# Performance work log

Hardware: AMD Instinct MI355X
Metric: run time of the kernel (lower is better)

## Reference

```python
import jax, jax.numpy as jnp
import numpy as np

B, C, K, P, H, W = 4, 128, 64, 8, 256, 256


def _img2patch(x, p):
    b, c, h, w = x.shape
    # [b,c,h,w] -> [b,c,p*p, (h//p)*(w//p)]
    return x.reshape(b, c, p, h // p, p, w // p).transpose(0, 1, 2, 4, 3, 5).reshape(b, c, p * p, -1)


def _patch2img(x, p, h, w):
    b, c = x.shape[:2]
    return x.reshape(b, c, p, p, h // p, w // p).transpose(0, 1, 2, 4, 3, 5).reshape(b, c, h, w)


def _conv1x1(x, Wm, bvec=None):
    # 1x1 conv on [b,c,pp,L] == channel matmul
    y = jnp.einsum('oc,bcpl->bopl', Wm, x)
    if bvec is not None:
        y = y + bvec[None, :, None, None]
    return y


def _l2norm(x, axis):
    return x / (1e-6 + jnp.sqrt(jnp.sum(x * x, axis=axis, keepdims=True)))


def setup_inputs():
    key = jax.random.key(0)
    ks = jax.random.split(key, 14)
    def wmat(k_, o, i):
        return jax.random.normal(k_, (o, i), jnp.float32) * np.float32(np.sqrt(2.0 / o))
    def bvec(k_, o):
        return jax.random.normal(k_, (o,), jnp.float32) * np.float32(0.01)
    return {
        'x1': jax.random.normal(ks[0], (B, C, H, W), jnp.float32),
        'x2': jax.random.normal(ks[1], (B, C, H, W), jnp.float32),
        'w_v': wmat(ks[2], K, 2 * C), 'b_v': bvec(ks[3], K),
        'w1_1': wmat(ks[4], C, C), 'b1_1': bvec(ks[5], C),
        'w2_1': wmat(ks[6], K, C), 'b2_1': bvec(ks[7], K),
        'w_out1': wmat(ks[8], C, C),
        'w1_2': wmat(ks[9], C, C), 'b1_2': bvec(ks[10], C),
        'w2_2': wmat(ks[11], K, C), 'b2_2': bvec(ks[12], K),
        'w_out2': wmat(ks[13], C, C),
        'p': P, 'k': K,
    }


def reference(x1, x2, w_v, b_v, w1_1, b1_1, w2_1, b2_1, w_out1, w1_2, b1_2, w2_2, b2_2, w_out2, p, k):
    b, c, h, w = x1.shape
    pp = p * p
    L = (h // p) * (w // p)
    bpp = b * pp
    x1p = _img2patch(x1, p)  # [b,c,pp,L]
    x2p = _img2patch(x2, p)
    y1_1 = _conv1x1(x1p, w1_1, b1_1).transpose(0, 2, 1, 3).reshape(bpp, c, L)
    y2_1 = _conv1x1(x1p, w2_1, b2_1).transpose(0, 2, 3, 1).reshape(bpp, L, k)
    y1_2 = _conv1x1(x2p, w1_2, b1_2).transpose(0, 2, 1, 3).reshape(bpp, c, L)
    y2_2 = _conv1x1(x2p, w2_2, b2_2).transpose(0, 2, 3, 1).reshape(bpp, L, k)
    v = _conv1x1(jnp.concatenate([x1p, x2p], axis=1), w_v, b_v)  # [b,k,pp,L]
    v = v.transpose(0, 2, 1, 3).reshape(bpp, k, L)
    v = jax.nn.softmax(v, axis=1)
    u1 = _l2norm(jnp.matmul(y1_1, y2_1), axis=1)  # [bpp,c,k]
    u2 = _l2norm(jnp.matmul(y1_2, y2_2), axis=1)
    y3_1 = jnp.matmul(u1, v).reshape(b, pp, c, L).transpose(0, 2, 1, 3)
    y3_2 = jnp.matmul(u2, v).reshape(b, pp, c, L).transpose(0, 2, 1, 3)
    out1 = jnp.einsum('oc,bchw->bohw', w_out1, _patch2img(y3_1, p, h, w))
    out2 = jnp.einsum('oc,bchw->bohw', w_out2, _patch2img(y3_2, p, h, w))
    return out1, out2
```

## Files before the change

kernel.cpp:

```cpp
#include <hip/hip_runtime.h>
#include <cstdint>

typedef __attribute__((ext_vector_type(8))) short short8;
typedef __attribute__((ext_vector_type(4))) float v4f;

#define B_ 4
#define C_ 128
#define K_ 64
#define H_ 256
#define W_ 256
#define HW_ (H_*W_)
#define L_ 1024
#define J_ 256
#define LC 128
#define NCH 8

#define OFF_WFH  0ull
#define OFF_WFL  131072ull
#define OFF_WOF  262144ull
#define OFF_BIAS 327680ull
#define OFF_VWS  335872ull
#define OFF_MFR  (OFF_VWS + 33554432ull)

static __device__ __forceinline__ unsigned short f2bf(float x) {
    unsigned u = __builtin_bit_cast(unsigned, x);
    unsigned r = (u + 0x7FFFu + ((u >> 16) & 1u)) >> 16;
    return (unsigned short)r;
}
static __device__ __forceinline__ float bf2f(unsigned short h) {
    unsigned u = ((unsigned)h) << 16;
    return __builtin_bit_cast(float, u);
}
static __device__ __forceinline__ v4f mfma16(short8 a, short8 b, v4f c) {
    return __builtin_amdgcn_mfma_f32_16x16x32_bf16(a, b, c, 0, 0, 0);
}

union U8 { unsigned short u[8]; short8 v; };

__global__ void prep_kernel(const float* __restrict__ w_v, const float* __restrict__ b_v,
                            const float* __restrict__ w1_1, const float* __restrict__ b1_1,
                            const float* __restrict__ w2_1, const float* __restrict__ b2_1,
                            const float* __restrict__ wout1,
                            const float* __restrict__ w1_2, const float* __restrict__ b1_2,
                            const float* __restrict__ w2_2, const float* __restrict__ b2_2,
                            const float* __restrict__ wout2,
                            char* __restrict__ wsb) {
    int tid = blockIdx.x * 256 + threadIdx.x;
    if (tid < 65536) {
        int jj = tid & 7, lane = (tid >> 3) & 63, kc = (tid >> 9) & 3;
        int omt = (tid >> 11) & 15, s = (tid >> 15) & 1;
        int o = omt * 16 + (lane & 15);
        int c = kc * 32 + ((lane >> 4) * 8) + jj;
        const float* w1 = s ? w1_2 : w1_1;
        const float* w2 = s ? w2_2 : w2_1;
        float v;
        if (o < 128)      v = w1[o * 128 + c];
        else if (o < 192) v = w2[(o - 128) * 128 + c];
        else              v = w_v[(o - 192) * 256 + s * 128 + c];
        unsigned short hi = f2bf(v);
        unsigned short lo = f2bf(v - bf2f(hi));
        ((unsigned short*)(wsb + OFF_WFH))[tid] = hi;
        ((unsigned short*)(wsb + OFF_WFL))[tid] = lo;
    } else if (tid < 98304) {
        int id = tid - 65536;
        int jj = id & 7, lane = (id >> 3) & 63, kc = (id >> 9) & 3;
        int om = (id >> 11) & 7, s = (id >> 14) & 1;
        int o = om * 16 + (lane & 15);
        int c = kc * 32 + ((lane >> 4) * 8) + jj;
        const float* wo = s ? wout2 : wout1;
        ((unsigned short*)(wsb + OFF_WOF))[id] = f2bf(wo[o * 128 + c]);
    } else if (tid < 98816) {
        int id = tid - 98304;
        int s = id >> 8, o = id & 255;
        const float* b1 = s ? b1_2 : b1_1;
        const float* b2 = s ? b2_2 : b2_1;
        float v;
        if (o < 128)      v = b1[o];
        else if (o < 192) v = b2[o - 128];
        else              v = b_v[o - 192];
        ((float*)(wsb + OFF_BIAS))[id] = v;
    }
}

__global__ __attribute__((amdgpu_flat_work_group_size(512, 512), amdgpu_waves_per_eu(2, 2)))
void fused_kernel(
    const float* __restrict__ x1, const float* __restrict__ x2,
    char* __restrict__ wsb) {
    __shared__ __align__(16) char smem[151040];
    unsigned short* Xfh = (unsigned short*)&smem[0];
    unsigned short* Xfl = (unsigned short*)&smem[32768];
    unsigned short* Y1b = (unsigned short*)&smem[65536];
    unsigned short* Y2b = (unsigned short*)&smem[100352];
    float*          LG  = (float*)&smem[117760];
    float*          UF  = (float*)&smem[0];
    unsigned short* UH  = (unsigned short*)&smem[100352];
    unsigned short* MB  = (unsigned short*)&smem[65536];

    const unsigned short* wfh = (const unsigned short*)(wsb + OFF_WFH);
    const unsigned short* wfl = (const unsigned short*)(wsb + OFF_WFL);
    const unsigned short* wof = (const unsigned short*)(wsb + OFF_WOF);
    const float* biasws = (const float*)(wsb + OFF_BIAS);
    unsigned short* vws = (unsigned short*)(wsb + OFF_VWS);
    unsigned short* mfr = (unsigned short*)(wsb + OFF_MFR);

    const int t = threadIdx.x;
    const int lane = t & 63;
    const int w = __builtin_amdgcn_readfirstlane(t >> 6);
    const int j = blockIdx.x;
    const int b = j >> 6, q = j & 63, i0 = q >> 3, i2 = q & 7;
    const long imgbase = (long)b * C_ * HW_ + (long)(i0 * 32) * W_ + i2 * 32;

    const int lquad = lane >> 4;
    const int lmod = lane & 15;

    float pb[2][2][4];
#pragma unroll
    for (int s = 0; s < 2; s++)
#pragma unroll
        for (int h = 0; h < 2; h++)
#pragma unroll
            for (int r = 0; r < 4; r++)
                pb[s][h][r] = biasws[s * 256 + w * 32 + h * 16 + lquad * 4 + r];

    v4f uacc[2][4];
#pragma unroll
    for (int s = 0; s < 2; s++)
#pragma unroll
        for (int kn = 0; kn < 4; kn++)
            uacc[s][kn] = (v4f){0.f, 0.f, 0.f, 0.f};

    const int dl = t & 127, c8 = t >> 7;
    const int srow = dl >> 5, scol = dl & 31;
    const int sln = dl >> 4, slp = dl & 15;

    float R[32];
#pragma unroll
    for (int p = 0; p < 4; p++)
#pragma unroll
        for (int jj = 0; jj < 8; jj++) {
            int c = (p * 4 + c8) * 8 + jj;
            R[p * 8 + jj] = x1[imgbase + (long)c * HW_ + srow * W_ + scol];
        }

    for (int lc = 0; lc < NCH; lc++) {
        v4f pacc[2][8];
#pragma unroll
        for (int s = 0; s < 2; s++) {
#pragma unroll
            for (int p = 0; p < 4; p++) {
                U8 hv, lv;
#pragma unroll
                for (int jj = 0; jj < 8; jj++) {
                    float v = R[p * 8 + jj];
                    unsigned short hh = f2bf(v);
                    hv.u[jj] = hh;
                    lv.u[jj] = f2bf(v - bf2f(hh));
                }
                int co = p * 4 + c8;
                int base = ((sln * 4 + (co >> 2)) * 64 + ((co & 3) * 16 + slp)) * 8;
                *(short8*)&Xfh[base] = hv.v;
                *(short8*)&Xfl[base] = lv.v;
            }
            __syncthreads();
            if (s == 0 || lc < NCH - 1) {
                const float* xp = s ? x1 : x2;
                const int nlc = s ? lc + 1 : lc;
#pragma unroll
                for (int p = 0; p < 4; p++)
#pragma unroll
                    for (int jj = 0; jj < 8; jj++) {
                        int c = (p * 4 + c8) * 8 + jj;
                        R[p * 8 + jj] = xp[imgbase + (long)c * HW_ + (nlc * 4 + srow) * W_ + scol];
                    }
            }
            if (s == 0 || w < 6) {
#pragma unroll
                for (int h = 0; h < 2; h++)
#pragma unroll
                    for (int ln = 0; ln < 8; ln++)
                        pacc[h][ln] = (v4f){pb[s][h][0], pb[s][h][1], pb[s][h][2], pb[s][h][3]};
            }
#pragma unroll
            for (int kc = 0; kc < 4; kc++) {
                int wi0 = (((s * 16 + (w * 2 + 0)) * 4 + kc) * 64 + lane) * 8;
                int wi1 = (((s * 16 + (w * 2 + 1)) * 4 + kc) * 64 + lane) * 8;
                short8 wh0 = *(const short8*)&wfh[wi0];
                short8 wh1 = *(const short8*)&wfh[wi1];
                short8 wlo0 = *(const short8*)&wfl[wi0];
                short8 wlo1 = *(const short8*)&wfl[wi1];
#pragma unroll
                for (int ln = 0; ln < 8; ln++) {
                    short8 bh = *(const short8*)&Xfh[((ln * 4 + kc) * 64 + lane) * 8];
                    short8 bl = *(const short8*)&Xfl[((ln * 4 + kc) * 64 + lane) * 8];
                    pacc[0][ln] = mfma16(wh0, bh, pacc[0][ln]);
                    pacc[0][ln] = mfma16(wlo0, bh, pacc[0][ln]);
                    pacc[0][ln] = mfma16(wh0, bl, pacc[0][ln]);
                    pacc[1][ln] = mfma16(wh1, bh, pacc[1][ln]);
                    pacc[1][ln] = mfma16(wlo1, bh, pacc[1][ln]);
                    pacc[1][ln] = mfma16(wh1, bl, pacc[1][ln]);
                }
            }
            if (w < 4) {
#pragma unroll
                for (int h = 0; h < 2; h++)
#pragma unroll
                    for (int ln = 0; ln < 8; ln++)
#pragma unroll
                        for (int r = 0; r < 4; r++)
                            Y1b[(w * 32 + h * 16 + lquad * 4 + r) * 136 + ln * 16 + lmod] = f2bf(pacc[h][ln][r]);
            } else if (w < 6) {
#pragma unroll
                for (int h = 0; h < 2; h++)
#pragma unroll
                    for (int ln = 0; ln < 8; ln++)
#pragma unroll
                        for (int r = 0; r < 4; r++)
                            Y2b[((w - 4) * 32 + h * 16 + lquad * 4 + r) * 136 + ln * 16 + lmod] = f2bf(pacc[h][ln][r]);
            } else if (s == 1) {
#pragma unroll
                for (int h = 0; h < 2; h++)
#pragma unroll
                    for (int ln = 0; ln < 8; ln++)
#pragma unroll
                        for (int r = 0; r < 4; r++)
                            LG[(ln * 16 + lmod) * 65 + (w - 6) * 32 + h * 16 + lquad * 4 + r] = pacc[h][ln][r];
            }
            __syncthreads();
#pragma unroll
            for (int kcl = 0; kcl < 4; kcl++) {
                short8 a = *(const short8*)&Y1b[(w * 16 + lmod) * 136 + kcl * 32 + lquad * 8];
#pragma unroll
                for (int kn = 0; kn < 4; kn++) {
                    short8 bb = *(const short8*)&Y2b[(kn * 16 + lmod) * 136 + kcl * 32 + lquad * 8];
                    uacc[s][kn] = mfma16(a, bb, uacc[s][kn]);
                }
            }
            if (s == 1) {
                if (t < 128) {
                    float* row = &LG[t * 65];
                    float mx = row[0];
#pragma unroll 8
                    for (int k = 1; k < 64; k++) mx = fmaxf(mx, row[k]);
                    float ssum = 0.f;
#pragma unroll 8
                    for (int k = 0; k < 64; k++) { float e = __expf(row[k] - mx); row[k] = e; ssum += e; }
                    float rs = 1.f / ssum;
#pragma unroll 8
                    for (int k = 0; k < 64; k++) row[k] *= rs;
                }
                __syncthreads();
                {
                    int l2 = t >> 2, kq = (t & 3) * 16;
                    U8 o1, o2;
#pragma unroll
                    for (int i = 0; i < 8; i++) o1.u[i] = f2bf(LG[l2 * 65 + kq + i]);
#pragma unroll
                    for (int i = 0; i < 8; i++) o2.u[i] = f2bf(LG[l2 * 65 + kq + 8 + i]);
                    unsigned long long vb = ((unsigned long long)j * 1024 + lc * 128 + l2) * 64 + kq;
                    *(short8*)&vws[vb] = o1.v;
                    *(short8*)&vws[vb + 8] = o2.v;
                }
            }
        }
    }

#pragma unroll
    for (int s = 0; s < 2; s++) {
        __syncthreads();
#pragma unroll
        for (int kn = 0; kn < 4; kn++)
#pragma unroll
            for (int r = 0; r < 4; r++)
                UF[(kn * 16 + lmod) * 133 + w * 16 + lquad * 4 + r] = uacc[s][kn][r];
        __syncthreads();
        if (t < 64) {
            const float* rp = &UF[t * 133];
            float ss = 0.f;
#pragma unroll 8
            for (int c = 0; c < 128; c++) ss += rp[c] * rp[c];
            UF[t * 133 + 128] = 1.f / (1e-6f + sqrtf(ss));
        }
        __syncthreads();
        {
            int kk = t >> 3, c0 = (t & 7) * 16;
            float rn = UF[kk * 133 + 128];
#pragma unroll
            for (int i = 0; i < 16; i++)
                UH[kk * 136 + c0 + i] = f2bf(UF[kk * 133 + c0 + i] * rn);
        }
        __syncthreads();
        v4f macc[4];
#pragma unroll
        for (int kn = 0; kn < 4; kn++) macc[kn] = (v4f){0.f, 0.f, 0.f, 0.f};
#pragma unroll
        for (int kc = 0; kc < 4; kc++) {
            short8 a = *(const short8*)&wof[(((s * 8 + w) * 4 + kc) * 64 + lane) * 8];
#pragma unroll
            for (int kn = 0; kn < 4; kn++) {
                short8 bb = *(const short8*)&UH[(kn * 16 + lmod) * 136 + kc * 32 + lquad * 8];
                macc[kn] = mfma16(a, bb, macc[kn]);
            }
        }
        __syncthreads();
#pragma unroll
        for (int kn = 0; kn < 4; kn++)
#pragma unroll
            for (int r = 0; r < 4; r++)
                MB[(w * 16 + lquad * 4 + r) * 72 + kn * 16 + lmod] = f2bf(macc[kn][r]);
        __syncthreads();
#pragma unroll
        for (int p = 0; p < 2; p++) {
            int id = p * 512 + t;
            int om = id >> 7, kc = (id >> 6) & 1, l2 = id & 63;
            short8 mv = *(const short8*)&MB[(om * 16 + (l2 & 15)) * 72 + kc * 32 + ((l2 >> 4) * 8)];
            *(short8*)&mfr[(((unsigned long long)j * 2 + s) * 1024 + id) * 8] = mv;
        }
    }
}

__global__ __launch_bounds__(512, 4) void out_kernel(const char* __restrict__ wsb,
                                                     float* __restrict__ out) {
    const unsigned short* vws = (const unsigned short*)(wsb + OFF_VWS);
    const unsigned short* mfr = (const unsigned short*)(wsb + OFF_MFR);
    const int t = threadIdx.x;
    const int lane = t & 63;
    const int w = __builtin_amdgcn_readfirstlane(t >> 6);
    const int j = blockIdx.x >> 2;
    const int slice = blockIdx.x & 3;
    const int b = j >> 6, q = j & 63, i0 = q >> 3, i2 = q & 7;
    const long obase = (long)b * C_ * HW_ + (long)(i0 * 32) * W_ + i2 * 32;
    const int lquad = lane >> 4, lmod = lane & 15;

    short8 afr[2][2];
#pragma unroll
    for (int s = 0; s < 2; s++)
#pragma unroll
        for (int kc = 0; kc < 2; kc++)
            afr[s][kc] = *(const short8*)&mfr[(((unsigned long long)j * 2 + s) * 1024 + (w * 2 + kc) * 64 + lane) * 8];

    const long orow = obase + (long)(w * 16 + lmod) * HW_;
#pragma unroll 4
    for (int i = 0; i < 16; i++) {
        int ln = slice * 16 + i;
        int l = ln * 16 + lmod;
        short8 b0  = *(const short8*)&vws[((unsigned long long)j * 1024 + l) * 64 + lquad * 8];
        short8 b1v = *(const short8*)&vws[((unsigned long long)j * 1024 + l) * 64 + 32 + lquad * 8];
        int lo = ln * 16 + lquad * 4;
        long base2 = orow + (long)(lo >> 5) * W_ + (lo & 31);
#pragma unroll
        for (int s = 0; s < 2; s++) {
            v4f acc = {0.f, 0.f, 0.f, 0.f};
            acc = mfma16(b0,  afr[s][0], acc);
            acc = mfma16(b1v, afr[s][1], acc);
            *(v4f*)&out[base2 + (long)s * B_ * C_ * HW_] = acc;
        }
    }
}

extern "C" void kernel_launch(void* const* d_in, const int* in_sizes, int n_in,
                              void* d_out, int out_size, void* d_ws, size_t ws_size,
                              hipStream_t stream) {
    (void)in_sizes; (void)n_in; (void)out_size; (void)ws_size;
    const float* x1    = (const float*)d_in[0];
    const float* x2    = (const float*)d_in[1];
    const float* w_v   = (const float*)d_in[2];
    const float* b_v   = (const float*)d_in[3];
    const float* w1_1  = (const float*)d_in[4];
    const float* b1_1  = (const float*)d_in[5];
    const float* w2_1  = (const float*)d_in[6];
    const float* b2_1  = (const float*)d_in[7];
    const float* wout1 = (const float*)d_in[8];
    const float* w1_2  = (const float*)d_in[9];
    const float* b1_2  = (const float*)d_in[10];
    const float* w2_2  = (const float*)d_in[11];
    const float* b2_2  = (const float*)d_in[12];
    const float* wout2 = (const float*)d_in[13];
    char* wsb  = (char*)d_ws;
    float* out = (float*)d_out;

    hipLaunchKernelGGL(prep_kernel, dim3(386), dim3(256), 0, stream,
                       w_v, b_v, w1_1, b1_1, w2_1, b2_1, wout1,
                       w1_2, b1_2, w2_2, b2_2, wout2, wsb);
    hipLaunchKernelGGL(fused_kernel, dim3(J_), dim3(512), 0, stream, x1, x2, wsb);
    hipLaunchKernelGGL(out_kernel, dim3(J_ * 4), dim3(512), 0, stream, wsb, out);
}
```

Before: 709.3 us.

## Fuse output projection kernel into fused kernel and parallelize softmax across lanes

Removes the separate out_kernel by keeping the per-patch M fragments in shared memory and computing the final outputs directly in the fused kernel. This drops the global round-trip of the M fragments and one kernel launch. The softmax also moves from 128 threads looping over 64 values to all 512 threads, four lanes per row combined with shuffles, which removes a barrier. In exchange, the output stage now runs on only 256 blocks instead of 1024, so writing the large output has less parallelism. The V values are still written to and read back from global memory inside the same kernel, ordered only by a threadfence.

Result: faster. 682.8 us (-3.7%).

```diff
diff --git a/kernel.cpp b/kernel.cpp
--- a/kernel.cpp
+++ b/kernel.cpp
@@ -20,7 +20,6 @@
 #define OFF_WOF  262144ull
 #define OFF_BIAS 327680ull
 #define OFF_VWS  335872ull
-#define OFF_MFR  (OFF_VWS + 33554432ull)
 
 static __device__ __forceinline__ unsigned short f2bf(float x) {
     unsigned u = __builtin_bit_cast(unsigned, x);
@@ -85,7 +84,7 @@
 __global__ __attribute__((amdgpu_flat_work_group_size(512, 512), amdgpu_waves_per_eu(2, 2)))
 void fused_kernel(
     const float* __restrict__ x1, const float* __restrict__ x2,
-    char* __restrict__ wsb) {
+    char* __restrict__ wsb, float* __restrict__ out) {
     __shared__ __align__(16) char smem[151040];
     unsigned short* Xfh = (unsigned short*)&smem[0];
     unsigned short* Xfl = (unsigned short*)&smem[32768];
@@ -101,7 +100,6 @@
     const unsigned short* wof = (const unsigned short*)(wsb + OFF_WOF);
     const float* biasws = (const float*)(wsb + OFF_BIAS);
     unsigned short* vws = (unsigned short*)(wsb + OFF_VWS);
-    unsigned short* mfr = (unsigned short*)(wsb + OFF_MFR);
 
     const int t = threadIdx.x;
     const int lane = t & 63;
@@ -236,33 +234,34 @@
                 }
             }
             if (s == 1) {
-                if (t < 128) {
-                    float* row = &LG[t * 65];
-                    float mx = row[0];
-#pragma unroll 8
-                    for (int k = 1; k < 64; k++) mx = fmaxf(mx, row[k]);
-                    float ssum = 0.f;
-#pragma unroll 8
-                    for (int k = 0; k < 64; k++) { float e = __expf(row[k] - mx); row[k] = e; ssum += e; }
-                    float rs = 1.f / ssum;
-#pragma unroll 8
-                    for (int k = 0; k < 64; k++) row[k] *= rs;
-                }
-                __syncthreads();
-                {
-                    int l2 = t >> 2, kq = (t & 3) * 16;
-                    U8 o1, o2;
-#pragma unroll
-                    for (int i = 0; i < 8; i++) o1.u[i] = f2bf(LG[l2 * 65 + kq + i]);
-#pragma unroll
-                    for (int i = 0; i < 8; i++) o2.u[i] = f2bf(LG[l2 * 65 + kq + 8 + i]);
-                    unsigned long long vb = ((unsigned long long)j * 1024 + lc * 128 + l2) * 64 + kq;
-                    *(short8*)&vws[vb] = o1.v;
-                    *(short8*)&vws[vb + 8] = o2.v;
-                }
+                int l2 = t >> 2, part = t & 3;
+                float vv[16];
+#pragma unroll
+                for (int i = 0; i < 16; i++) vv[i] = LG[l2 * 65 + part * 16 + i];
+                float mx = vv[0];
+#pragma unroll
+                for (int i = 1; i < 16; i++) mx = fmaxf(mx, vv[i]);
+                mx = fmaxf(mx, __shfl_xor(mx, 1));
+                mx = fmaxf(mx, __shfl_xor(mx, 2));
+                float ssum = 0.f;
+#pragma unroll
+                for (int i = 0; i < 16; i++) { float e = __expf(vv[i] - mx); vv[i] = e; ssum += e; }
+                ssum += __shfl_xor(ssum, 1);
+                ssum += __shfl_xor(ssum, 2);
+                float rs = 1.f / ssum;
+                U8 o1, o2;
+#pragma unroll
+                for (int i = 0; i < 8; i++) o1.u[i] = f2bf(vv[i] * rs);
+#pragma unroll
+                for (int i = 0; i < 8; i++) o2.u[i] = f2bf(vv[8 + i] * rs);
+                unsigned long long vb = ((unsigned long long)j * 1024 + lc * 128 + l2) * 64 + part * 16;
+                *(short8*)&vws[vb] = o1.v;
+                *(short8*)&vws[vb + 8] = o2.v;
             }
         }
     }
+
+    __threadfence();
 
 #pragma unroll
     for (int s = 0; s < 2; s++) {
@@ -308,51 +307,22 @@
             for (int r = 0; r < 4; r++)
                 MB[(w * 16 + lquad * 4 + r) * 72 + kn * 16 + lmod] = f2bf(macc[kn][r]);
         __syncthreads();
-#pragma unroll
-        for (int p = 0; p < 2; p++) {
-            int id = p * 512 + t;
-            int om = id >> 7, kc = (id >> 6) & 1, l2 = id & 63;
-            short8 mv = *(const short8*)&MB[(om * 16 + (l2 & 15)) * 72 + kc * 32 + ((l2 >> 4) * 8)];
-            *(short8*)&mfr[(((unsigned long long)j * 2 + s) * 1024 + id) * 8] = mv;
-        }
-    }
-}
-
-__global__ __launch_bounds__(512, 4) void out_kernel(const char* __restrict__ wsb,
-                                                     float* __restrict__ out) {
-    const unsigned short* vws = (const unsigned short*)(wsb + OFF_VWS);
-    const unsigned short* mfr = (const unsigned short*)(wsb + OFF_MFR);
-    const int t = threadIdx.x;
-    const int lane = t & 63;
-    const int w = __builtin_amdgcn_readfirstlane(t >> 6);
-    const int j = blockIdx.x >> 2;
-    const int slice = blockIdx.x & 3;
-    const int b = j >> 6, q = j & 63, i0 = q >> 3, i2 = q & 7;
-    const long obase = (long)b * C_ * HW_ + (long)(i0 * 32) * W_ + i2 * 32;
-    const int lquad = lane >> 4, lmod = lane & 15;
-
-    short8 afr[2][2];
-#pragma unroll
-    for (int s = 0; s < 2; s++)
+        short8 mfrag[2];
 #pragma unroll
         for (int kc = 0; kc < 2; kc++)
-            afr[s][kc] = *(const short8*)&mfr[(((unsigned long long)j * 2 + s) * 1024 + (w * 2 + kc) * 64 + lane) * 8];
-
-    const long orow = obase + (long)(w * 16 + lmod) * HW_;
+            mfrag[kc] = *(const short8*)&MB[(w * 16 + lmod) * 72 + kc * 32 + lquad * 8];
+        const long orow = (long)b * C_ * HW_ + (long)(i0 * 32) * W_ + i2 * 32
+                        + (long)(w * 16 + lmod) * HW_ + (long)s * B_ * C_ * HW_;
 #pragma unroll 4
-    for (int i = 0; i < 16; i++) {
-        int ln = slice * 16 + i;
-        int l = ln * 16 + lmod;
-        short8 b0  = *(const short8*)&vws[((unsigned long long)j * 1024 + l) * 64 + lquad * 8];
-        short8 b1v = *(const short8*)&vws[((unsigned long long)j * 1024 + l) * 64 + 32 + lquad * 8];
-        int lo = ln * 16 + lquad * 4;
-        long base2 = orow + (long)(lo >> 5) * W_ + (lo & 31);
-#pragma unroll
-        for (int s = 0; s < 2; s++) {
+        for (int ln = 0; ln < 64; ln++) {
+            int l = ln * 16 + lmod;
+            short8 b0  = *(const short8*)&vws[((unsigned long long)j * 1024 + l) * 64 + lquad * 8];
+            short8 b1v = *(const short8*)&vws[((unsigned long long)j * 1024 + l) * 64 + 32 + lquad * 8];
+            int lo = ln * 16 + lquad * 4;
             v4f acc = {0.f, 0.f, 0.f, 0.f};
-            acc = mfma16(b0,  afr[s][0], acc);
-            acc = mfma16(b1v, afr[s][1], acc);
-            *(v4f*)&out[base2 + (long)s * B_ * C_ * HW_] = acc;
+            acc = mfma16(b0,  mfrag[0], acc);
+            acc = mfma16(b1v, mfrag[1], acc);
+            *(v4f*)&out[orow + (long)(lo >> 5) * W_ + (lo & 31)] = acc;
         }
     }
 }
@@ -381,6 +351,5 @@
     hipLaunchKernelGGL(prep_kernel, dim3(386), dim3(256), 0, stream,
                        w_v, b_v, w1_1, b1_1, w2_1, b2_1, wout1,
                        w1_2, b1_2, w2_2, b2_2, wout2, wsb);
-    hipLaunchKernelGGL(fused_kernel, dim3(J_), dim3(512), 0, stream, x1, x2, wsb);
-    hipLaunchKernelGGL(out_kernel, dim3(J_ * 4), dim3(512), 0, stream, wsb, out);
-}
+    hipLaunchKernelGGL(fused_kernel, dim3(J_), dim3(512), 0, stream, x1, x2, wsb, out);
+}
```
